# Kernel tuning notes

Hardware: AMD Instinct MI355X
Metric: run time of the kernel (lower is better)

## Reference

```python
import jax, jax.numpy as jnp
import numpy as np

B, T, D_IN, E, H = 2, 2048, 1024, 64, 16  # batch, num_tokens, input dim, emb_size(per-head), num_heads


def setup_inputs() -> dict:
    key = jax.random.key(0)
    ks = jax.random.split(key, 6)
    s = 0.02
    inp = jax.random.normal(ks[0], (B, T, D_IN), dtype=jnp.float32)
    # causal mask: 1.0 where attention is disallowed (j > i), matching `scaled_compat -= mask * 1e9`
    mask = jnp.triu(jnp.ones((T, T), dtype=jnp.float32), k=1)
    Wq = jax.random.normal(ks[1], (D_IN, E * H), dtype=jnp.float32) * s
    Wk = jax.random.normal(ks[2], (D_IN, E * H), dtype=jnp.float32) * s
    Wv = jax.random.normal(ks[3], (D_IN, E * H), dtype=jnp.float32) * s
    Wu = jax.random.normal(ks[4], (E * H, E), dtype=jnp.float32) * s
    bu = jnp.zeros((E,), dtype=jnp.float32)
    return {"inp": inp, "mask": mask, "Wq": Wq, "Wk": Wk, "Wv": Wv, "Wu": Wu, "bu": bu}


def reference(inp, mask, Wq, Wk, Wv, Wu, bu):
    b = inp.shape[0]
    q = inp @ Wq  # [B,T,E*H]
    k = inp @ Wk
    v = inp @ Wv
    # NOTE: original reshapes last dim as (E, H) -> heads on fastest axis (interleaved layout)
    q = q.reshape(b, T, E, H)
    k = k.reshape(b, T, E, H)
    v = v.reshape(b, T, E, H)
    scores = jnp.einsum("bteh,bseh->bhts", q, k) / jnp.sqrt(jnp.float32(E))  # [B,H,T,T]
    if mask is not None:
        scores = scores - mask * 1e9
    attn = jax.nn.softmax(scores, axis=-1)
    wv = jnp.einsum("bhts,bseh->bhte", attn, v)  # [B,H,T,E]
    # transpose [0,2,3,1] -> [B,T,E,H], then flatten to [B,T,E*H] (H fastest, matching original)
    wv = jnp.transpose(wv, (0, 2, 3, 1)).reshape(b, T, E * H)
    return wv @ Wu + bu  # unify Dense(emb_size), with bias
```

## Files before the change

### kernel.cpp

```cpp
#include <hip/hip_runtime.h>


typedef __bf16 bf16x8 __attribute__((ext_vector_type(8)));
typedef float f32x4 __attribute__((ext_vector_type(4)));
typedef unsigned short u16;
typedef unsigned int u32;

#define AS1 __attribute__((address_space(1)))
#define AS3 __attribute__((address_space(3)))

__device__ __forceinline__ void gll16(const void* g, void* l) {
    __builtin_amdgcn_global_load_lds((const AS1 u32*)g, (AS3 u32*)l, 16, 0, 0);
}

__device__ __forceinline__ u16 f2bf(float f) {
    union { float f; u32 u; } v; v.f = f;
    u32 r = (v.u + 0x7FFFu + ((v.u >> 16) & 1u)) >> 16;
    return (u16)r;
}

#define MM 4096
#define SCALE_LOG2E 0.18033688011112042f

__global__ void cast_x(const float* __restrict__ in, u16* __restrict__ out, int n4) {
    int i = blockIdx.x * blockDim.x + threadIdx.x;
    if (i < n4) {
        float4 f = ((const float4*)in)[i];
        ushort4 o;
        o.x = f2bf(f.x); o.y = f2bf(f.y); o.z = f2bf(f.z); o.w = f2bf(f.w);
        ((ushort4*)out)[i] = o;
    }
}

__global__ void transpose_w(const float* __restrict__ Wq, const float* __restrict__ Wk,
                            const float* __restrict__ Wv, const float* __restrict__ Wu,
                            u16* __restrict__ wqt, u16* __restrict__ wkt,
                            u16* __restrict__ wvt, u16* __restrict__ wut) {
    int z = blockIdx.z;
    const float* src; u16* dst; int N;
    if (z == 0)      { src = Wq; dst = wqt; N = 1024; }
    else if (z == 1) { src = Wk; dst = wkt; N = 1024; }
    else if (z == 2) { src = Wv; dst = wvt; N = 1024; }
    else             { src = Wu; dst = wut; N = 64; if (blockIdx.y >= 2) return; }
    __shared__ float lds[32][33];
    int k0 = blockIdx.x * 32, n0 = blockIdx.y * 32;
    int tid = threadIdx.x;
    int c = tid & 31, r0 = tid >> 5;
#pragma unroll
    for (int p = 0; p < 4; ++p) {
        int r = r0 + p * 8;
        lds[r][c] = src[(k0 + r) * N + n0 + c];
    }
    __syncthreads();
#pragma unroll
    for (int p = 0; p < 4; ++p) {
        int n = n0 + r0 + p * 8;
        if (z < 3) {
            int rnew = ((n & 15) << 6) | (n >> 4);
            dst[rnew * 1024 + k0 + c] = f2bf(lds[c][n - n0]);
        } else {
            int k = k0 + c;
            int kp = ((k & 15) << 6) | (k >> 4);
            dst[n * 1024 + kp] = f2bf(lds[c][n - n0]);
        }
    }
}

__global__ __launch_bounds__(256) void gemm_qkv(const u16* __restrict__ xb,
                                                const u16* __restrict__ wqt,
                                                const u16* __restrict__ wkt,
                                                const u16* __restrict__ wvt,
                                                u16* __restrict__ qh, u16* __restrict__ kh,
                                                u16* __restrict__ vh) {
    int z = blockIdx.z;
    const u16* wt = (z == 0) ? wqt : (z == 1) ? wkt : wvt;
    u16* dst      = (z == 0) ? qh  : (z == 1) ? kh  : vh;
    __shared__ u16 lA[2][128 * 32];
    __shared__ u16 lB[2][128 * 32];
    int tid = threadIdx.x;
    int m0 = blockIdx.x * 128, n0 = blockIdx.y * 128;
    int lane = tid & 63, w = tid >> 6;
    int wr = w >> 1, wc = w & 1;
    int l15 = lane & 15, quad = lane >> 4;
    f32x4 acc[4][4] = {};
    int srow = tid >> 2, scol = (tid & 3) * 8;
    const u16* ga = xb + (m0 + srow) * 1024 + scol;
    const u16* gb = wt + (n0 + srow) * 1024 + scol;
#pragma unroll
    for (int pp = 0; pp < 2; ++pp) {
        gll16(ga + pp * 65536, lA[0] + (pp * 256 + tid) * 8);
        gll16(gb + pp * 65536, lB[0] + (pp * 256 + tid) * 8);
    }
#pragma unroll 1
    for (int kk = 0; kk < 32; ++kk) {
        int cur = kk & 1;
        asm volatile("s_waitcnt vmcnt(0)" ::: "memory");
        __builtin_amdgcn_s_barrier();
        if (kk + 1 < 32) {
            int kb = (kk + 1) * 32;
#pragma unroll
            for (int pp = 0; pp < 2; ++pp) {
                gll16(ga + pp * 65536 + kb, lA[cur ^ 1] + (pp * 256 + tid) * 8);
                gll16(gb + pp * 65536 + kb, lB[cur ^ 1] + (pp * 256 + tid) * 8);
            }
        }
        bf16x8 af[4], bfr[4];
#pragma unroll
        for (int i = 0; i < 4; ++i)
            af[i] = *(const bf16x8*)(lA[cur] + (wr * 64 + i * 16 + l15) * 32 + quad * 8);
#pragma unroll
        for (int j = 0; j < 4; ++j)
            bfr[j] = *(const bf16x8*)(lB[cur] + (wc * 64 + j * 16 + l15) * 32 + quad * 8);
#pragma unroll
        for (int i = 0; i < 4; ++i)
#pragma unroll
            for (int j = 0; j < 4; ++j)
                acc[i][j] = __builtin_amdgcn_mfma_f32_16x16x32_bf16(af[i], bfr[j], acc[i][j], 0, 0, 0);
    }
    int bb = m0 >> 11;
    int hb = (n0 >> 6) + wc;
    if (z < 2) {
        float scale = (z == 0) ? SCALE_LOG2E : 1.f;
#pragma unroll
        for (int i = 0; i < 4; ++i)
#pragma unroll
            for (int j = 0; j < 4; ++j)
#pragma unroll
                for (int r = 0; r < 4; ++r) {
                    int m = m0 + wr * 64 + i * 16 + quad * 4 + r;
                    dst[m * 1024 + hb * 64 + j * 16 + l15] = f2bf(acc[i][j][r] * scale);
                }
    } else {
#pragma unroll
        for (int i = 0; i < 4; ++i)
#pragma unroll
            for (int j = 0; j < 4; ++j) {
                int t4 = (m0 & 2047) + wr * 64 + i * 16 + quad * 4;
                ushort4 o;
                o.x = f2bf(acc[i][j][0]); o.y = f2bf(acc[i][j][1]);
                o.z = f2bf(acc[i][j][2]); o.w = f2bf(acc[i][j][3]);
                *(ushort4*)(dst + (((bb * 16 + hb) * 64) + j * 16 + l15) * 2048 + t4) = o;
            }
    }
}

__global__ __launch_bounds__(256) void attn(const u16* __restrict__ qh, const u16* __restrict__ kh,
                                            const u16* __restrict__ vh, u16* __restrict__ ot) {
    __shared__ u16 smem[12800];
    u16* sQ = smem;
    u16* sK = smem + 4608;
    u16* sV = smem + 8704;
    const int tid = threadIdx.x;
    const int lane = tid & 63, w = tid >> 6;
    const int quad = lane >> 4, l15 = lane & 15;
    const int by = blockIdx.y;
    const int qt = (blockIdx.x + by) & 31;
    const int b = by >> 4, h = by & 15;
    const u16* qbase = qh + (b * 2048) * 1024 + h * 64;
    const u16* kbase = kh + (b * 2048) * 1024 + h * 64;
    const u16* vbase = vh + (by * 64) * 2048;
    const int c0 = tid, c1 = 256 + tid;
    const int r0c = c0 >> 3, o0c = (c0 & 7) * 8;
    const int r1c = c1 >> 3, o1c = (c1 & 7) * 8;
    const int sw0 = ((r0c >> 1) & 3) << 3;
    const int sw1 = ((r1c >> 1) & 3) << 3;
    u16* sKd0 = sK + (o0c >> 5) * 2048 + r0c * 32 + ((o0c & 31) ^ sw0);
    u16* sKd1 = sK + (o1c >> 5) * 2048 + r1c * 32 + ((o1c & 31) ^ sw1);
    u16* sVd0 = sV + (o0c >> 5) * 2048 + r0c * 32 + ((o0c & 31) ^ sw0);
    u16* sVd1 = sV + (o1c >> 5) * 2048 + r1c * 32 + ((o1c & 31) ^ sw1);
    const u16* kg0 = kbase + r0c * 1024 + o0c;
    const u16* kg1 = kbase + r1c * 1024 + o1c;
    const u16* vg0 = vbase + r0c * 2048 + o0c;
    const u16* vg1 = vbase + r1c * 2048 + o1c;
    const int qsw = (quad ^ ((l15 >> 1) & 3)) * 8;

    gll16(qbase + (qt * 64 + r0c) * 1024 + o0c, sQ + c0 * 8);
    gll16(qbase + (qt * 64 + r1c) * 1024 + o1c, sQ + c1 * 8);
    __syncthreads();
    bf16x8 aq[2];
    aq[0] = *(const bf16x8*)(sQ + (w * 16 + l15) * 64 + quad * 8);
    aq[1] = *(const bf16x8*)(sQ + (w * 16 + l15) * 64 + 32 + quad * 8);
    float lpart[4] = {0.f, 0.f, 0.f, 0.f};
    f32x4 oacc[4] = {};
    const int nj = qt + 1;
    uint4 kr0 = *(const uint4*)(kg0);
    uint4 kr1 = *(const uint4*)(kg1);
    uint4 vr0 = *(const uint4*)(vg0);
    uint4 vr1 = *(const uint4*)(vg1);
    for (int jt = 0; jt < nj; ++jt) {
        __syncthreads();
        *(uint4*)sKd0 = kr0; *(uint4*)sKd1 = kr1;
        *(uint4*)sVd0 = vr0; *(uint4*)sVd1 = vr1;
        __syncthreads();
        if (jt + 1 < nj) {
            kr0 = *(const uint4*)(kg0 + (jt + 1) * 65536);
            kr1 = *(const uint4*)(kg1 + (jt + 1) * 65536);
            vr0 = *(const uint4*)(vg0 + (jt + 1) * 64);
            vr1 = *(const uint4*)(vg1 + (jt + 1) * 64);
        }
        f32x4 sacc[4] = {};
#pragma unroll
        for (int j4 = 0; j4 < 4; ++j4)
#pragma unroll
            for (int k2 = 0; k2 < 2; ++k2) {
                bf16x8 bk = *(const bf16x8*)(sK + k2 * 2048 + (j4 * 16 + l15) * 32 + qsw);
                sacc[j4] = __builtin_amdgcn_mfma_f32_16x16x32_bf16(aq[k2], bk, sacc[j4], 0, 0, 0);
            }
        if (jt == qt) {
#pragma unroll
            for (int j4 = 0; j4 < 4; ++j4)
#pragma unroll
                for (int r = 0; r < 4; ++r) {
                    int sg = j4 * 16 + l15;
                    int tg = w * 16 + quad * 4 + r;
                    if (sg > tg) sacc[j4][r] = -1e30f;
                }
        }
#pragma unroll
        for (int j4 = 0; j4 < 4; ++j4)
#pragma unroll
            for (int r = 0; r < 4; ++r) {
                float pe = __builtin_amdgcn_exp2f(sacc[j4][r]);
                sacc[j4][r] = pe;
                lpart[r] += pe;
            }
        u16* sP = sQ;
#pragma unroll
        for (int j4 = 0; j4 < 4; ++j4)
#pragma unroll
            for (int r = 0; r < 4; ++r)
                sP[(w * 16 + quad * 4 + r) * 72 + j4 * 16 + l15] = f2bf(sacc[j4][r]);
        bf16x8 ap[2];
        ap[0] = *(const bf16x8*)(sP + (w * 16 + l15) * 72 + quad * 8);
        ap[1] = *(const bf16x8*)(sP + (w * 16 + l15) * 72 + 32 + quad * 8);
#pragma unroll
        for (int e4 = 0; e4 < 4; ++e4)
#pragma unroll
            for (int k2 = 0; k2 < 2; ++k2) {
                bf16x8 bv = *(const bf16x8*)(sV + k2 * 2048 + (e4 * 16 + l15) * 32 + qsw);
                oacc[e4] = __builtin_amdgcn_mfma_f32_16x16x32_bf16(ap[k2], bv, oacc[e4], 0, 0, 0);
            }
    }
#pragma unroll
    for (int r = 0; r < 4; ++r) {
        float rs = lpart[r];
#pragma unroll
        for (int off = 1; off < 16; off <<= 1) rs += __shfl_xor(rs, off, 16);
        float inv = 1.f / rs;
        int t = qt * 64 + w * 16 + quad * 4 + r;
        int base = (b * 2048 + t) * 1024 + h * 64;
#pragma unroll
        for (int e4 = 0; e4 < 4; ++e4)
            ot[base + e4 * 16 + l15] = f2bf(oacc[e4][r] * inv);
    }
}

__global__ __launch_bounds__(256) void gemm_out(const u16* __restrict__ ot, const u16* __restrict__ wut,
                                                const float* __restrict__ bu, float* __restrict__ out) {
    __shared__ float red[4][1088];
    int tid = threadIdx.x, lane = tid & 63, w = tid >> 6;
    int quad = lane >> 4, l15 = lane & 15;
    int m0 = blockIdx.x * 16;
    f32x4 acc[4] = {};
    const u16* aptr = ot + (m0 + l15) * 1024 + w * 256 + quad * 8;
    const u16* bptr = wut + l15 * 1024 + w * 256 + quad * 8;
#pragma unroll
    for (int kk = 0; kk < 8; ++kk) {
        bf16x8 af = *(const bf16x8*)(aptr + kk * 32);
#pragma unroll
        for (int j = 0; j < 4; ++j) {
            bf16x8 bfr = *(const bf16x8*)(bptr + j * 16 * 1024 + kk * 32);
            acc[j] = __builtin_amdgcn_mfma_f32_16x16x32_bf16(af, bfr, acc[j], 0, 0, 0);
        }
    }
#pragma unroll
    for (int j = 0; j < 4; ++j)
#pragma unroll
        for (int r = 0; r < 4; ++r)
            red[w][(j * 16 + l15) * 17 + quad * 4 + r] = acc[j][r];
    __syncthreads();
    int n = tid & 63, mq = tid >> 6;
    float bias = bu[n];
#pragma unroll
    for (int i = 0; i < 4; ++i) {
        int m = mq * 4 + i;
        float s = red[0][n * 17 + m] + red[1][n * 17 + m] + red[2][n * 17 + m] + red[3][n * 17 + m];
        out[(m0 + m) * 64 + n] = s + bias;
    }
}

#define OFF_XB   0u
#define OFF_WQT  8388608u
#define OFF_WKT  10485760u
#define OFF_WVT  12582912u
#define OFF_WUT  14680064u
#define OFF_QH   14811136u
#define OFF_KH   23199744u
#define OFF_VH   31588352u
#define OFF_OT   OFF_XB

extern "C" void kernel_launch(void* const* d_in, const int* in_sizes, int n_in,
                              void* d_out, int out_size, void* d_ws, size_t ws_size,
                              hipStream_t stream) {
    (void)in_sizes; (void)n_in; (void)out_size; (void)ws_size;
    const float* inp = (const float*)d_in[0];
    const float* Wq = (const float*)d_in[2];
    const float* Wk = (const float*)d_in[3];
    const float* Wv = (const float*)d_in[4];
    const float* Wu = (const float*)d_in[5];
    const float* bu = (const float*)d_in[6];
    float* out = (float*)d_out;
    char* ws = (char*)d_ws;
    u16* xb  = (u16*)(ws + OFF_XB);
    u16* wqt = (u16*)(ws + OFF_WQT);
    u16* wkt = (u16*)(ws + OFF_WKT);
    u16* wvt = (u16*)(ws + OFF_WVT);
    u16* wut = (u16*)(ws + OFF_WUT);
    u16* qh  = (u16*)(ws + OFF_QH);
    u16* kh  = (u16*)(ws + OFF_KH);
    u16* vh  = (u16*)(ws + OFF_VH);
    u16* ot  = (u16*)(ws + OFF_OT);

    cast_x<<<4096, 256, 0, stream>>>(inp, xb, (MM * 1024) / 4);
    transpose_w<<<dim3(32, 32, 4), 256, 0, stream>>>(Wq, Wk, Wv, Wu, wqt, wkt, wvt, wut);
    gemm_qkv<<<dim3(32, 8, 3), 256, 0, stream>>>(xb, wqt, wkt, wvt, qh, kh, vh);
    attn<<<dim3(32, 32), 256, 0, stream>>>(qh, kh, vh, ot);
    gemm_out<<<256, 256, 0, stream>>>(ot, wut, bu, out);
}
```

Measured before the change: 188.9 us.

## Split long causal query tiles across two blocks and combine partial outputs

```diff
diff --git a/kernel.cpp b/kernel.cpp
--- a/kernel.cpp
+++ b/kernel.cpp
@@ -144,8 +144,9 @@
     }
 }
 
-__global__ __launch_bounds__(256) void attn(const u16* __restrict__ qh, const u16* __restrict__ kh,
-                                            const u16* __restrict__ vh, u16* __restrict__ ot) {
+__global__ __launch_bounds__(256, 8) void attn(const u16* __restrict__ qh, const u16* __restrict__ kh,
+                                               const u16* __restrict__ vh, u16* __restrict__ ot,
+                                               float* __restrict__ part, float* __restrict__ lp) {
     __shared__ u16 smem[12800];
     u16* sQ = smem;
     u16* sK = smem + 4608;
@@ -153,8 +154,11 @@
     const int tid = threadIdx.x;
     const int lane = tid & 63, w = tid >> 6;
     const int quad = lane >> 4, l15 = lane & 15;
-    const int by = blockIdx.y;
-    const int qt = (blockIdx.x + by) & 31;
+    const int s = blockIdx.x, by = blockIdx.y;
+    int qt, j0, j1, half;
+    if (s < 16)      { qt = 15 - s;  j0 = 0;             j1 = qt + 1;        half = -1; }
+    else if (s < 32) { qt = s;       j0 = 0;             j1 = (qt + 1) >> 1; half = 0;  }
+    else             { qt = s - 16;  j0 = (qt + 1) >> 1; j1 = qt + 1;        half = 1;  }
     const int b = by >> 4, h = by & 15;
     const u16* qbase = qh + (b * 2048) * 1024 + h * 64;
     const u16* kbase = kh + (b * 2048) * 1024 + h * 64;
@@ -182,17 +186,16 @@
     aq[1] = *(const bf16x8*)(sQ + (w * 16 + l15) * 64 + 32 + quad * 8);
     float lpart[4] = {0.f, 0.f, 0.f, 0.f};
     f32x4 oacc[4] = {};
-    const int nj = qt + 1;
-    uint4 kr0 = *(const uint4*)(kg0);
-    uint4 kr1 = *(const uint4*)(kg1);
-    uint4 vr0 = *(const uint4*)(vg0);
-    uint4 vr1 = *(const uint4*)(vg1);
-    for (int jt = 0; jt < nj; ++jt) {
+    uint4 kr0 = *(const uint4*)(kg0 + j0 * 65536);
+    uint4 kr1 = *(const uint4*)(kg1 + j0 * 65536);
+    uint4 vr0 = *(const uint4*)(vg0 + j0 * 64);
+    uint4 vr1 = *(const uint4*)(vg1 + j0 * 64);
+    for (int jt = j0; jt < j1; ++jt) {
         __syncthreads();
         *(uint4*)sKd0 = kr0; *(uint4*)sKd1 = kr1;
         *(uint4*)sVd0 = vr0; *(uint4*)sVd1 = vr1;
         __syncthreads();
-        if (jt + 1 < nj) {
+        if (jt + 1 < j1) {
             kr0 = *(const uint4*)(kg0 + (jt + 1) * 65536);
             kr1 = *(const uint4*)(kg1 + (jt + 1) * 65536);
             vr0 = *(const uint4*)(vg0 + (jt + 1) * 64);
@@ -241,17 +244,59 @@
                 oacc[e4] = __builtin_amdgcn_mfma_f32_16x16x32_bf16(ap[k2], bv, oacc[e4], 0, 0, 0);
             }
     }
-#pragma unroll
-    for (int r = 0; r < 4; ++r) {
-        float rs = lpart[r];
-#pragma unroll
-        for (int off = 1; off < 16; off <<= 1) rs += __shfl_xor(rs, off, 16);
-        float inv = 1.f / rs;
-        int t = qt * 64 + w * 16 + quad * 4 + r;
-        int base = (b * 2048 + t) * 1024 + h * 64;
-#pragma unroll
-        for (int e4 = 0; e4 < 4; ++e4)
-            ot[base + e4 * 16 + l15] = f2bf(oacc[e4][r] * inv);
+    if (half < 0) {
+#pragma unroll
+        for (int r = 0; r < 4; ++r) {
+            float rs = lpart[r];
+#pragma unroll
+            for (int off = 1; off < 16; off <<= 1) rs += __shfl_xor(rs, off, 16);
+            float inv = 1.f / rs;
+            int t = qt * 64 + w * 16 + quad * 4 + r;
+            int base = (b * 2048 + t) * 1024 + h * 64;
+#pragma unroll
+            for (int e4 = 0; e4 < 4; ++e4)
+                ot[base + e4 * 16 + l15] = f2bf(oacc[e4][r] * inv);
+        }
+    } else {
+        int pb = by * 16 + (qt - 16);
+        float* pg = part + (pb * 2 + half) * 4096;
+        float* lg = lp + pb * 128 + half * 64;
+#pragma unroll
+        for (int r = 0; r < 4; ++r) {
+            float rs = lpart[r];
+#pragma unroll
+            for (int off = 1; off < 16; off <<= 1) rs += __shfl_xor(rs, off, 16);
+            int row = w * 16 + quad * 4 + r;
+            if (l15 == 0) lg[row] = rs;
+#pragma unroll
+            for (int e4 = 0; e4 < 4; ++e4)
+                pg[row * 64 + e4 * 16 + l15] = oacc[e4][r];
+        }
+    }
+}
+
+__global__ __launch_bounds__(256) void combine_o(const float* __restrict__ part,
+                                                 const float* __restrict__ lp,
+                                                 u16* __restrict__ ot) {
+    int pb = blockIdx.x, tid = threadIdx.x;
+    int by = pb >> 4, qt = 16 + (pb & 15);
+    int b = by >> 4, h = by & 15;
+    const float* pA = part + pb * 8192;
+    const float* pB = pA + 4096;
+    const float* lA = lp + pb * 128;
+    const float* lB = lA + 64;
+#pragma unroll
+    for (int p = 0; p < 4; ++p) {
+        int e = p * 1024 + tid * 4;
+        int row = e >> 6, col = e & 63;
+        float4 a = *(const float4*)(pA + e);
+        float4 c = *(const float4*)(pB + e);
+        float inv = 1.f / (lA[row] + lB[row]);
+        int t = qt * 64 + row;
+        ushort4 o;
+        o.x = f2bf((a.x + c.x) * inv); o.y = f2bf((a.y + c.y) * inv);
+        o.z = f2bf((a.z + c.z) * inv); o.w = f2bf((a.w + c.w) * inv);
+        *(ushort4*)(ot + (b * 2048 + t) * 1024 + h * 64 + col) = o;
     }
 }
 
@@ -298,6 +343,8 @@
 #define OFF_KH   23199744u
 #define OFF_VH   31588352u
 #define OFF_OT   OFF_XB
+#define OFF_PART 39976960u
+#define OFF_LP   56754176u
 
 extern "C" void kernel_launch(void* const* d_in, const int* in_sizes, int n_in,
                               void* d_out, int out_size, void* d_ws, size_t ws_size,
@@ -320,10 +367,13 @@
     u16* kh  = (u16*)(ws + OFF_KH);
     u16* vh  = (u16*)(ws + OFF_VH);
     u16* ot  = (u16*)(ws + OFF_OT);
+    float* part = (float*)(ws + OFF_PART);
+    float* lpw  = (float*)(ws + OFF_LP);
 
     cast_x<<<4096, 256, 0, stream>>>(inp, xb, (MM * 1024) / 4);
     transpose_w<<<dim3(32, 32, 4), 256, 0, stream>>>(Wq, Wk, Wv, Wu, wqt, wkt, wvt, wut);
     gemm_qkv<<<dim3(32, 8, 3), 256, 0, stream>>>(xb, wqt, wkt, wvt, qh, kh, vh);
-    attn<<<dim3(32, 32), 256, 0, stream>>>(qh, kh, vh, ot);
+    attn<<<dim3(48, 32), 256, 0, stream>>>(qh, kh, vh, ot, part, lpw);
+    combine_o<<<512, 256, 0, stream>>>(part, lpw, ot);
     gemm_out<<<256, 256, 0, stream>>>(ot, wut, bu, out);
 }
```

Measured after the change: 193.8 us. 2.6% more time.
